# Optimization experiments

Hardware: AMD Instinct MI355X
Metric: run time of the kernel (lower is better)

The kernel has to match this reference:

```python
import jax, jax.numpy as jnp
import numpy as np

E, B, N, F, F1D, H, L, H2, PE_DIM = 4, 16384, 1024, 64, 64, 256, 2, 256, 63
TOPK_MEM = 16      # self.top_K: memory retrieval top-k
W0_SIREN = 30.0    # SIREN omega_0 for 'sine' nonlinearity
NUM_FREQ = 10      # PosEncoding num_frequencies
LINE_DIM = 64      # feat_shapes[0]


def _ln(h, g, b):
    m = jnp.mean(h, axis=-1, keepdims=True)
    v = jnp.mean((h - m) ** 2, axis=-1, keepdims=True)
    return (h - m) / jnp.sqrt(v + 1e-5) * g + b


def _pos_enc(coords):
    # NeRF positional encoding: [coords, sin/cos interleaved per coord per freq]
    freqs = 2.0 ** jnp.arange(NUM_FREQ, dtype=coords.dtype)
    scaled = coords[..., None] * freqs * jnp.pi            # (B, 3, NF)
    sc = jnp.stack([jnp.sin(scaled), jnp.cos(scaled)], axis=-1)  # (B, 3, NF, 2)
    return jnp.concatenate([coords, sc.reshape(coords.shape[0], -1)], axis=-1)  # (B, 63)


def _forward(x, lines, mem_k, mem_v, enc_w0, enc_b0, enc_wh, enc_bh, enc_wo, enc_bo,
             ln_g, ln_b, wq, wk, wv, ad_w0, ad_b0, ad_w1, ad_b1, ad_ln_g, ad_ln_b,
             mg_w0, mg_b0, mg_w1, mg_b1, fw0, fb0, fw1, fb1, fw2, fb2, fw3, fb3, route_k):
    coords = x[:, :3]
    # --- 1D line feature interpolation (param_feats) ---
    p = x[:, 3] * (LINE_DIM - 1)
    pf = jnp.floor(p)
    w = p - pf
    il = pf.astype(jnp.int32)
    ih = jnp.clip(pf + 1.0, 0.0, LINE_DIM - 1).astype(jnp.int32)
    f1d = lines[0][:, il] + w * (lines[0][:, ih] - lines[0][:, il])  # (F1D, B)
    param_feats = f1d.T                                              # (B, F1D)

    pe_x = _pos_enc(coords)                                          # (B, 63)
    scale = float(F) ** 0.5

    def expert(ew0, eb0, ewh, ebh, ewo, ebo, wq_e, wk_e, wv_e, mk, mv,
               aw0, ab0, aw1, ab1, ag, ab):
        # SIREN encoder MLP
        h = jnp.sin(W0_SIREN * (pe_x @ ew0 + eb0))
        for l in range(L):
            h = jnp.sin(W0_SIREN * (h @ ewh[l] + ebh[l]))
        mlp_feats = h @ ewo + ebo                          # (B, F)
        q = _ln(mlp_feats, ln_g, ln_b) @ wq_e              # (B, F)
        kp = mk @ wk_e                                     # (N, F) precomputed keys
        vp = mv @ wv_e                                     # (N, F) precomputed values
        scores = q @ kp.T                                  # (B, N)
        _, idx = jax.lax.top_k(scores, TOPK_MEM)           # (B, K)
        k_top = kp[idx]                                    # (B, K, F)
        v_top = vp[idx]                                    # (B, K, F)
        pfe = jnp.broadcast_to(param_feats[:, None, :], (param_feats.shape[0], TOPK_MEM, F1D))
        a = jnp.concatenate([v_top, pfe], axis=-1)         # (B, K, F+F1D)
        a = jax.nn.relu(a @ aw0 + ab0) @ aw1 + ab1
        adapted = v_top + _ln(a, ag, ab)
        attn = jax.nn.softmax(jnp.einsum('bf,bkf->bk', q, k_top) / scale, axis=-1)
        return jnp.einsum('bk,bkf->bf', attn, adapted) + mlp_feats

    # compute every expert densely (vectorized), then gather routed top-k outputs
    all_out = jax.vmap(expert)(enc_w0, enc_b0, enc_wh, enc_bh, enc_wo, enc_bo,
                               wq, wk, wv, mem_k, mem_v,
                               ad_w0, ad_b0, ad_w1, ad_b1, ad_ln_g, ad_ln_b)  # (E, B, F)

    raw_q = jax.nn.relu(coords @ mg_w0 + mg_b0) @ mg_w1 + mg_b1   # manager_net (B, E)
    probs = jnp.clip(jax.nn.softmax(raw_q, axis=-1), 1e-8, None)
    vals, tidx = jax.lax.top_k(probs, route_k)                    # (B, k)
    vals = vals / jnp.sum(vals, axis=-1, keepdims=True)
    gathered = jnp.take_along_axis(jnp.swapaxes(all_out, 0, 1), tidx[..., None], axis=1)  # (B, k, F)
    spatial = jnp.sum(vals[..., None] * gathered, axis=1)         # (B, F)

    h = jax.nn.relu(spatial @ fw0 + fb0)
    h = jax.nn.relu(h @ fw1 + fb1)
    h = jax.nn.relu(h @ fw2 + fb2)
    refined = jax.nn.sigmoid(h @ fw3 + fb3)
    return refined, raw_q


def setup_inputs() -> dict:
    ks = jax.random.split(jax.random.key(0), 24)
    f32 = jnp.float32
    rn = lambda i, shp, s: jax.random.normal(ks[i], shp, f32) * s
    xav = lambda fi, fo: (2.0 / (fi + fo)) ** 0.5
    return {
        'x': jax.random.uniform(ks[0], (B, 4), f32),
        'lines': jax.random.uniform(ks[1], (1, F1D, LINE_DIM), f32, 0.7, 0.8),
        'mem_k': rn(2, (E, N, F), 1.0),
        'mem_v': rn(3, (E, N, F), 1e-3),
        'enc_w0': rn(4, (E, PE_DIM, H), xav(PE_DIM, H)),
        'enc_b0': jnp.zeros((E, H), f32),
        'enc_wh': rn(5, (E, L, H, H), xav(H, H)),
        'enc_bh': jnp.zeros((E, L, H), f32),
        'enc_wo': rn(6, (E, H, F), xav(H, F)),
        'enc_bo': jnp.zeros((E, F), f32),
        'ln_g': jnp.ones((F,), f32),
        'ln_b': jnp.zeros((F,), f32),
        'wq': rn(7, (E, F, F), xav(F, F)),
        'wk': rn(8, (E, F, F), xav(F, F)),
        'wv': rn(9, (E, F, F), xav(F, F)),
        'ad_w0': rn(10, (E, F + F1D, 64), xav(F + F1D, 64)),
        'ad_b0': rn(11, (E, 64), 1e-3),
        'ad_w1': rn(12, (E, 64, F), xav(64, F)),
        'ad_b1': rn(13, (E, F), 1e-3),
        'ad_ln_g': jnp.ones((E, F), f32),
        'ad_ln_b': jnp.zeros((E, F), f32),
        'mg_w0': rn(14, (3, 64), 0.5),
        'mg_b0': jnp.zeros((64,), f32),
        'mg_w1': rn(15, (64, E), 0.5),
        'mg_b1': jnp.zeros((E,), f32),
        'fw0': rn(16, (F, H2), xav(F, H2)),
        'fb0': rn(17, (H2,), 1e-3),
        'fw1': rn(18, (H2, H2), xav(H2, H2)),
        'fb1': rn(19, (H2,), 1e-3),
        'fw2': rn(20, (H2, H2), xav(H2, H2)),
        'fb2': rn(21, (H2,), 1e-3),
        'fw3': rn(22, (H2, 1), xav(H2, 1)),
        'fb3': rn(23, (1,), 1e-3),
        'route_k': 2,
    }


def reference(x, lines, mem_k, mem_v, enc_w0, enc_b0, enc_wh, enc_bh, enc_wo, enc_bo,
              ln_g, ln_b, wq, wk, wv, ad_w0, ad_b0, ad_w1, ad_b1, ad_ln_g, ad_ln_b,
              mg_w0, mg_b0, mg_w1, mg_b1, fw0, fb0, fw1, fb1, fw2, fb2, fw3, fb3, route_k):
    return _forward(x, lines, mem_k, mem_v, enc_w0, enc_b0, enc_wh, enc_bh, enc_wo, enc_bo,
                    ln_g, ln_b, wq, wk, wv, ad_w0, ad_b0, ad_w1, ad_b1, ad_ln_g, ad_ln_b,
                    mg_w0, mg_b0, mg_w1, mg_b1, fw0, fb0, fw1, fb1, fw2, fb2, fw3, fb3, route_k)
```

## Files before the change

kernel.cpp:

```cpp
#include <hip/hip_runtime.h>
#include <math.h>

#define EE 4
#define BB 16384
#define NN 1024
#define FF 64
#define HH 256
#define PED 63
#define TOPK 16
#define LINE 64
#define TS 32
#define NBX (BB/TS)
#define TSA 64
#define NBA 256

#define OFF_KP   0u
#define OFF_VP   262144u
#define OFF_VPA  524288u
#define OFF_PE   786432u
#define OFF_PF   1818624u
#define OFF_EO   2867200u
#define OFF_RW   4964352u
#define OFF_CNT  4997120u
#define OFF_LIST 4997128u
#define OFF_QV   5062664u
#define OFF_SM   7159816u
#define OFF_WP   OFF_EO

__device__ __forceinline__ float wred_sum(float v) {
#pragma unroll
    for (int off = 32; off > 0; off >>= 1) v += __shfl_xor(v, off, 64);
    return v;
}
__device__ __forceinline__ void wred_sum2(float& a, float& b) {
#pragma unroll
    for (int off = 32; off > 0; off >>= 1) {
        a += __shfl_xor(a, off, 64);
        b += __shfl_xor(b, off, 64);
    }
}

__global__ __launch_bounds__(256) void k_prep(
    const float* __restrict__ wv, const float* __restrict__ aw0,
    float* __restrict__ wp)
{
    int e = blockIdx.x;
    __shared__ float sa[FF*FF];
    for (int i = threadIdx.x; i < FF*FF; i += 256)
        sa[i] = aw0[(size_t)e*128*FF + i];
    __syncthreads();
    int f = threadIdx.x & 63, dg = threadIdx.x >> 6;
    for (int d = dg; d < FF; d += 4) {
        const float* wr = wv + (size_t)e*FF*FF + d*FF;
        float a = 0.f;
        for (int c = 0; c < FF; ++c) a = fmaf(wr[c], sa[c*FF+f], a);
        wp[(size_t)e*FF*FF + d*FF + f] = a;
    }
}

__global__ __launch_bounds__(256) void k_proj(
    const float* __restrict__ mem_k, const float* __restrict__ mem_v,
    const float* __restrict__ wk, const float* __restrict__ wv,
    const float* __restrict__ wp,
    float* __restrict__ kp, float* __restrict__ vp, float* __restrict__ vpa)
{
    int e = blockIdx.x >> 6;
    int nbase = (blockIdx.x & 63) * 16;
    __shared__ float swk[FF*FF], swv[FF*FF], swp[FF*FF];
    for (int i = threadIdx.x; i < FF*FF; i += 256) {
        swk[i] = wk[(size_t)e*FF*FF + i];
        swv[i] = wv[(size_t)e*FF*FF + i];
        swp[i] = wp[(size_t)e*FF*FF + i];
    }
    __syncthreads();
    int r4 = threadIdx.x >> 6;
    int f  = threadIdx.x & 63;
#pragma unroll 1
    for (int it = 0; it < 4; ++it) {
        int n = nbase + it*4 + r4;
        const float* mk = mem_k + ((size_t)e*NN + n)*FF;
        const float* mv = mem_v + ((size_t)e*NN + n)*FF;
        float ak = 0.f, av = 0.f, aa = 0.f;
#pragma unroll 1
        for (int c4 = 0; c4 < 16; ++c4) {
            float4 k4 = *(const float4*)&mk[4*c4];
            float4 v4 = *(const float4*)&mv[4*c4];
#pragma unroll
            for (int kk = 0; kk < 4; ++kk) {
                float mkc = (kk==0)?k4.x:((kk==1)?k4.y:((kk==2)?k4.z:k4.w));
                float mvc = (kk==0)?v4.x:((kk==1)?v4.y:((kk==2)?v4.z:v4.w));
                int c = 4*c4 + kk;
                ak = fmaf(mkc, swk[c*FF+f], ak);
                av = fmaf(mvc, swv[c*FF+f], av);
                aa = fmaf(mvc, swp[c*FF+f], aa);
            }
        }
        kp [((size_t)e*NN+n)*FF + f] = ak;
        vp [((size_t)e*NN+n)*FF + f] = av;
        vpa[((size_t)e*NN+n)*FF + f] = aa;
    }
}

__global__ __launch_bounds__(256) void k_route(
    const float* __restrict__ x, const float* __restrict__ lines,
    const float* __restrict__ mg_w0, const float* __restrict__ mg_b0,
    const float* __restrict__ mg_w1, const float* __restrict__ mg_b1,
    float* __restrict__ pe_x, float* __restrict__ pfm,
    float* __restrict__ rawq, float* __restrict__ rw,
    int* __restrict__ counts, int* __restrict__ lists)
{
    __shared__ float slines[LINE*LINE];
    for (int i = threadIdx.x; i < LINE*LINE; i += 256) slines[i] = lines[i];
    __syncthreads();
    int b = blockIdx.x*256 + threadIdx.x;
    float4 xx = ((const float4*)x)[b];
    float c0 = xx.x, c1 = xx.y, c2 = xx.z, c3 = xx.w;

    float p = c3 * (float)(LINE-1);
    float pfl = floorf(p);
    float w = p - pfl;
    int il = (int)pfl;
    int ih = (int)fminf(fmaxf(pfl + 1.f, 0.f), (float)(LINE-1));
    for (int c = 0; c < FF; ++c) {
        float lo = slines[c*LINE+il], hi = slines[c*LINE+ih];
        pfm[(size_t)b*FF + c] = lo + w*(hi-lo);
    }
    float* pe = pe_x + (size_t)b*PED;
    pe[0]=c0; pe[1]=c1; pe[2]=c2;
    const float PI = 3.14159265358979323846f;
    float coords[3] = {c0,c1,c2};
#pragma unroll
    for (int cc = 0; cc < 3; ++cc) {
        float fr = PI;
        for (int k = 0; k < 10; ++k) {
            float s = coords[cc]*fr;
            pe[3 + cc*20 + k*2 + 0] = sinf(s);
            pe[3 + cc*20 + k*2 + 1] = cosf(s);
            fr *= 2.f;
        }
    }
    float acc[4] = {mg_b1[0], mg_b1[1], mg_b1[2], mg_b1[3]};
    for (int j = 0; j < 64; ++j) {
        float h = fmaf(c0, mg_w0[j], fmaf(c1, mg_w0[64+j], fmaf(c2, mg_w0[128+j], mg_b0[j])));
        h = fmaxf(h, 0.f);
#pragma unroll
        for (int e4 = 0; e4 < 4; ++e4) acc[e4] = fmaf(h, mg_w1[j*4+e4], acc[e4]);
    }
#pragma unroll
    for (int e4 = 0; e4 < 4; ++e4) rawq[(size_t)b*4 + e4] = acc[e4];
    float m = fmaxf(fmaxf(acc[0],acc[1]), fmaxf(acc[2],acc[3]));
    float ex[4], den = 0.f;
#pragma unroll
    for (int e4 = 0; e4 < 4; ++e4) { ex[e4] = expf(acc[e4]-m); den += ex[e4]; }
    float pr[4];
#pragma unroll
    for (int e4 = 0; e4 < 4; ++e4) pr[e4] = fmaxf(ex[e4]/den, 1e-8f);
    int i0 = 0;
#pragma unroll
    for (int e4 = 1; e4 < 4; ++e4) if (pr[e4] > pr[i0]) i0 = e4;
    int i1 = -1;
#pragma unroll
    for (int e4 = 0; e4 < 4; ++e4) {
        if (e4 == i0) continue;
        if (i1 < 0 || pr[e4] > pr[i1]) i1 = e4;
    }
    float vs = pr[i0] + pr[i1];
    rw[b*2+0] = pr[i0]/vs;
    rw[b*2+1] = pr[i1]/vs;
    int p0 = atomicAdd(&counts[i0], 1);
    lists[i0*BB + p0] = b*2 + 0;
    int p1 = atomicAdd(&counts[i1], 1);
    lists[i1*BB + p1] = b*2 + 1;
}

__global__ __launch_bounds__(512, 3) void k_mlp(
    const float* __restrict__ pe_x,
    const float* __restrict__ enc_w0, const float* __restrict__ enc_b0,
    const float* __restrict__ enc_wh, const float* __restrict__ enc_bh,
    const float* __restrict__ enc_wo, const float* __restrict__ enc_bo,
    const float* __restrict__ ln_g, const float* __restrict__ ln_b,
    const float* __restrict__ wq,
    const int* __restrict__ counts, const int* __restrict__ lists,
    float* __restrict__ qv, float* __restrict__ smlpw)
{
    const int e = blockIdx.y;
    const int base = blockIdx.x * TS;
    const int cnt = counts[e];
    if (base >= cnt) return;

    __shared__ float sh[TS*HH];
    __shared__ float swt[4096];
    __shared__ int   slist[TS];

    const int tid = threadIdx.x;
    const int lane = tid & 63;
    const int wv = tid >> 6;
    const int r0 = wv*4;

    if (tid < TS) {
        int idx = base + tid;
        if (idx >= cnt) idx = cnt - 1;
        slist[tid] = lists[e*BB + idx];
    }
    __syncthreads();
    for (int i = tid; i < TS*64; i += 512) {
        int s = i >> 6, j = i & 63;
        int bq = slist[s] >> 1;
        sh[s*HH + j] = (j < PED) ? pe_x[(size_t)bq*PED + j] : 0.f;
    }

    float acc[4][4];

    {
        const float* W = enc_w0 + (size_t)e*PED*HH;
#pragma unroll
        for (int s = 0; s < 4; ++s)
#pragma unroll
            for (int j = 0; j < 4; ++j) acc[s][j] = 0.f;
#pragma unroll 1
        for (int t = 0; t < 4; ++t) {
            int rbase = t*16;
            int rows = (PED - rbase < 16) ? (PED - rbase) : 16;
            int total = rows*HH;
            __syncthreads();
            for (int i = tid*4; i < total; i += 2048)
                *(float4*)&swt[i] = *(const float4*)&W[rbase*HH + i];
            __syncthreads();
#pragma unroll 1
            for (int k = 0; k < rows; ++k) {
                float4 w4 = *(const float4*)&swt[k*HH + 4*lane];
#pragma unroll
                for (int s = 0; s < 4; ++s) {
                    float hv = sh[(r0+s)*HH + rbase + k];
                    acc[s][0] = fmaf(hv, w4.x, acc[s][0]);
                    acc[s][1] = fmaf(hv, w4.y, acc[s][1]);
                    acc[s][2] = fmaf(hv, w4.z, acc[s][2]);
                    acc[s][3] = fmaf(hv, w4.w, acc[s][3]);
                }
            }
        }
        __syncthreads();
        float4 b4 = *(const float4*)&enc_b0[e*HH + 4*lane];
#pragma unroll
        for (int s = 0; s < 4; ++s) {
            float4 o;
            o.x = sinf(30.0f*(acc[s][0] + b4.x));
            o.y = sinf(30.0f*(acc[s][1] + b4.y));
            o.z = sinf(30.0f*(acc[s][2] + b4.z));
            o.w = sinf(30.0f*(acc[s][3] + b4.w));
            *(float4*)&sh[(r0+s)*HH + 4*lane] = o;
        }
    }

#pragma unroll 1
    for (int layer = 0; layer < 2; ++layer) {
        const float* W = enc_wh + ((size_t)(e*2+layer))*HH*HH;
#pragma unroll
        for (int s = 0; s < 4; ++s)
#pragma unroll
            for (int j = 0; j < 4; ++j) acc[s][j] = 0.f;
#pragma unroll 1
        for (int t = 0; t < 16; ++t) {
            __syncthreads();
            for (int i = tid*4; i < 4096; i += 2048)
                *(float4*)&swt[i] = *(const float4*)&W[t*16*HH + i];
            __syncthreads();
#pragma unroll 1
            for (int k4 = 0; k4 < 4; ++k4) {
                float4 h4[4];
#pragma unroll
                for (int s = 0; s < 4; ++s)
                    h4[s] = *(const float4*)&sh[(r0+s)*HH + t*16 + 4*k4];
#pragma unroll
                for (int kk = 0; kk < 4; ++kk) {
                    float4 w4 = *(const float4*)&swt[(4*k4+kk)*HH + 4*lane];
#pragma unroll
                    for (int s = 0; s < 4; ++s) {
                        float hv = (kk==0)?h4[s].x:((kk==1)?h4[s].y:((kk==2)?h4[s].z:h4[s].w));
                        acc[s][0] = fmaf(hv, w4.x, acc[s][0]);
                        acc[s][1] = fmaf(hv, w4.y, acc[s][1]);
                        acc[s][2] = fmaf(hv, w4.z, acc[s][2]);
                        acc[s][3] = fmaf(hv, w4.w, acc[s][3]);
                    }
                }
            }
        }
        __syncthreads();
        float4 b4 = *(const float4*)&enc_bh[(e*2+layer)*HH + 4*lane];
#pragma unroll
        for (int s = 0; s < 4; ++s) {
            float4 o;
            o.x = sinf(30.0f*(acc[s][0] + b4.x));
            o.y = sinf(30.0f*(acc[s][1] + b4.y));
            o.z = sinf(30.0f*(acc[s][2] + b4.z));
            o.w = sinf(30.0f*(acc[s][3] + b4.w));
            *(float4*)&sh[(r0+s)*HH + 4*lane] = o;
        }
    }

    float smlp_r[4];
    {
        const float* W = enc_wo + (size_t)e*HH*FF;
        float a2o[4] = {0.f,0.f,0.f,0.f};
#pragma unroll 1
        for (int t = 0; t < 4; ++t) {
            __syncthreads();
            for (int i = tid*4; i < 4096; i += 2048)
                *(float4*)&swt[i] = *(const float4*)&W[t*64*FF + i];
            __syncthreads();
#pragma unroll 1
            for (int k4 = 0; k4 < 16; ++k4) {
                float4 h4[4];
#pragma unroll
                for (int s = 0; s < 4; ++s)
                    h4[s] = *(const float4*)&sh[(r0+s)*HH + t*64 + 4*k4];
#pragma unroll
                for (int kk = 0; kk < 4; ++kk) {
                    float w = swt[(4*k4+kk)*FF + lane];
#pragma unroll
                    for (int s = 0; s < 4; ++s) {
                        float hv = (kk==0)?h4[s].x:((kk==1)?h4[s].y:((kk==2)?h4[s].z:h4[s].w));
                        a2o[s] = fmaf(hv, w, a2o[s]);
                    }
                }
            }
        }
        float bv = enc_bo[e*FF + lane];
#pragma unroll
        for (int s = 0; s < 4; ++s) smlp_r[s] = a2o[s] + bv;
    }

    {
        const float* Wq = wq + (size_t)e*FF*FF;
        __syncthreads();
        for (int i = tid*4; i < 4096; i += 2048)
            *(float4*)&swt[i] = *(const float4*)&Wq[i];
        __syncthreads();
        float g = ln_g[lane], bb2 = ln_b[lane];
#pragma unroll 1
        for (int s = 0; s < 4; ++s) {
            float hv = smlp_r[s];
            float sm = hv, s2 = hv*hv;
            wred_sum2(sm, s2);
            float mean = sm * (1.f/64.f);
            float var = s2 * (1.f/64.f) - mean*mean;
            float lnv = (hv - mean) * rsqrtf(var + 1e-5f) * g + bb2;
            sh[(r0+s)*HH + lane] = lnv;
            float qa = 0.f;
#pragma unroll 1
            for (int c4 = 0; c4 < 16; ++c4) {
                float4 l4 = *(const float4*)&sh[(r0+s)*HH + 4*c4];
                qa = fmaf(l4.x, swt[(4*c4+0)*FF + lane], qa);
                qa = fmaf(l4.y, swt[(4*c4+1)*FF + lane], qa);
                qa = fmaf(l4.z, swt[(4*c4+2)*FF + lane], qa);
                qa = fmaf(l4.w, swt[(4*c4+3)*FF + lane], qa);
            }
            if (base + r0 + s < cnt) {
                size_t entry = (size_t)slist[r0+s];
                qv[entry*FF + lane] = qa;
                smlpw[entry*FF + lane] = smlp_r[s];
            }
        }
    }
}

__global__ __launch_bounds__(1024, 1) void k_attn(
    const float* __restrict__ pfm,
    const float* __restrict__ kp, const float* __restrict__ vp,
    const float* __restrict__ vpa,
    const float* __restrict__ qv, const float* __restrict__ smlpw,
    const float* __restrict__ aw0, const float* __restrict__ ab0,
    const float* __restrict__ aw1, const float* __restrict__ ab1,
    const float* __restrict__ adg, const float* __restrict__ adb,
    const int* __restrict__ counts, const int* __restrict__ lists,
    float* __restrict__ eo)
{
    const int e = blockIdx.y;
    const int base = blockIdx.x * TSA;
    const int cnt = counts[e];
    if (base >= cnt) return;

    __shared__ float su[16384];
    __shared__ float sa0[4096];
    __shared__ float sw1[4096];
    __shared__ int   slist[TSA];

    float* sq  = su;
    float* skp = su + 4096;

    const int tid = threadIdx.x;
    const int lane = tid & 63;
    const int wv = tid >> 6;
    const int r0 = wv*4;

    if (tid < TSA) {
        int idx = base + tid;
        if (idx >= cnt) idx = cnt - 1;
        slist[tid] = lists[e*BB + idx];
    }
    __syncthreads();
    {
        int s4 = tid >> 4, c4 = (tid & 15)*4;
        *(float4*)&sq[s4*64 + c4] = *(const float4*)&qv[(size_t)slist[s4]*FF + c4];
        const float* a0bG = aw0 + ((size_t)e*128 + 64)*FF;
        const float* w1G  = aw1 + (size_t)e*FF*FF;
        *(float4*)&sa0[tid*4] = *(const float4*)&a0bG[tid*4];
        *(float4*)&sw1[tid*4] = *(const float4*)&w1G[tid*4];
    }

    float sc[4][16];
    {
        const float* kpe = kp + (size_t)e*NN*FF;
        const int str = tid >> 4;
        const int stc = (tid & 15) * 4;
#pragma unroll 1
        for (int c = 0; c < 16; ++c) {
            __syncthreads();
            *(float4*)&skp[str*68 + stc] =
                *(const float4*)&kpe[(size_t)(c*64 + str)*FF + stc];
            __syncthreads();
            float a0 = 0.f, a1 = 0.f, a2s = 0.f, a3 = 0.f;
#pragma unroll
            for (int f4 = 0; f4 < 16; ++f4) {
                float4 k4 = *(const float4*)&skp[lane*68 + 4*f4];
                float4 q0 = *(const float4*)&sq[(r0+0)*64 + 4*f4];
                float4 q1 = *(const float4*)&sq[(r0+1)*64 + 4*f4];
                float4 q2 = *(const float4*)&sq[(r0+2)*64 + 4*f4];
                float4 q3 = *(const float4*)&sq[(r0+3)*64 + 4*f4];
                a0 = fmaf(k4.x,q0.x,fmaf(k4.y,q0.y,fmaf(k4.z,q0.z,fmaf(k4.w,q0.w,a0))));
                a1 = fmaf(k4.x,q1.x,fmaf(k4.y,q1.y,fmaf(k4.z,q1.z,fmaf(k4.w,q1.w,a1))));
                a2s= fmaf(k4.x,q2.x,fmaf(k4.y,q2.y,fmaf(k4.z,q2.z,fmaf(k4.w,q2.w,a2s))));
                a3 = fmaf(k4.x,q3.x,fmaf(k4.y,q3.y,fmaf(k4.z,q3.z,fmaf(k4.w,q3.w,a3))));
            }
            sc[0][c]=a0; sc[1][c]=a1; sc[2][c]=a2s; sc[3][c]=a3;
        }
    }
    __syncthreads();

    const float* vpe  = vp  + (size_t)e*NN*FF;
    const float* vpae = vpa + (size_t)e*NN*FF;
    const float agv = adg[e*FF + lane], abv = adb[e*FF + lane];
    const float ab0v = ab0[e*FF + lane];
    const float ab1v = ab1[e*FF + lane];
    float* plw = &su[wv*1024];

#pragma unroll
    for (int u = 0; u < 4; ++u) {
        int s = r0 + u;
        int entry = slist[s];
        int bq = entry >> 1;

        float pp = ab0v;
        {
            const float* pfr = pfm + (size_t)bq*FF;
#pragma unroll 1
            for (int c4 = 0; c4 < 16; ++c4) {
                float4 p4 = *(const float4*)&pfr[4*c4];
                pp = fmaf(p4.x, sa0[(4*c4+0)*FF + lane], pp);
                pp = fmaf(p4.y, sa0[(4*c4+1)*FF + lane], pp);
                pp = fmaf(p4.z, sa0[(4*c4+2)*FF + lane], pp);
                pp = fmaf(p4.w, sa0[(4*c4+3)*FF + lane], pp);
            }
        }

        int rns[16];
        float wrs[16];
        unsigned taken = 0u;
        bool need = true;
        float bv = -1e30f; int bn = 0x7fffffff;
        float v0max = 0.f, wsum = 0.f;
#pragma unroll
        for (int r = 0; r < TOPK; ++r) {
            if (need) {
                bv = -1e30f; bn = 0x7fffffff;
#pragma unroll
                for (int c = 0; c < 16; ++c) {
                    float v = sc[u][c];
                    int n = c*64 + lane;
                    bool ok = !((taken >> c) & 1u);
                    bool better = ok && (v > bv || (v == bv && n < bn));
                    bv = better ? v : bv;
                    bn = better ? n : bn;
                }
                need = false;
            }
            float rv = bv; int rn = bn;
#pragma unroll
            for (int off = 32; off > 0; off >>= 1) {
                float ov = __shfl_xor(rv, off, 64);
                int on = __shfl_xor(rn, off, 64);
                bool better = (ov > rv) || (ov == rv && on < rn);
                rv = better ? ov : rv;
                rn = better ? on : rn;
            }
            int rn_u = __builtin_amdgcn_readfirstlane(rn);
            if (r == 0) v0max = rv;
            float wr = expf((rv - v0max) * 0.125f);
            wsum += wr;
            if ((rn_u & 63) == lane) { taken |= 1u << (rn_u >> 6); need = true; }
            rns[r] = rn_u;
            wrs[r] = wr;
        }

        float oaccv = 0.f;
#pragma unroll
        for (int g2 = 0; g2 < 2; ++g2) {
            float pav[8], vv[8];
#pragma unroll
            for (int r8 = 0; r8 < 8; ++r8) {
                int r = g2*8 + r8;
                pav[r8] = vpae[(size_t)rns[r]*FF + lane];
                vv[r8]  = vpe [(size_t)rns[r]*FF + lane];
            }
#pragma unroll
            for (int r8 = 0; r8 < 8; ++r8)
                oaccv = fmaf(wrs[g2*8 + r8], vv[r8], oaccv);
#pragma unroll
            for (int q = 0; q < 2; ++q) {
                int qq = g2*2 + q;
                int slot = qq ^ (lane & 3);
                float4 o;
                o.x = fmaxf(pav[4*q+0] + pp, 0.f);
                o.y = fmaxf(pav[4*q+1] + pp, 0.f);
                o.z = fmaxf(pav[4*q+2] + pp, 0.f);
                o.w = fmaxf(pav[4*q+3] + pp, 0.f);
                *(float4*)&plw[lane*16 + slot*4] = o;
            }
        }
        float a2[16];
#pragma unroll
        for (int r = 0; r < 16; ++r) a2[r] = ab1v;
#pragma unroll 1
        for (int j4 = 0; j4 < 16; ++j4) {
            const float* plj = &plw[j4*64];
#pragma unroll
            for (int jj = 0; jj < 4; ++jj) {
                float w = sw1[(4*j4+jj)*FF + lane];
#pragma unroll
                for (int lq = 0; lq < 4; ++lq) {
                    float4 d = *(const float4*)&plj[jj*16 + ((lq ^ jj) * 4)];
                    a2[4*lq+0] = fmaf(d.x, w, a2[4*lq+0]);
                    a2[4*lq+1] = fmaf(d.y, w, a2[4*lq+1]);
                    a2[4*lq+2] = fmaf(d.z, w, a2[4*lq+2]);
                    a2[4*lq+3] = fmaf(d.w, w, a2[4*lq+3]);
                }
            }
        }
        float oln = 0.f;
#pragma unroll
        for (int r = 0; r < TOPK; ++r) {
            float av = a2[r];
            float sm = av, s2 = av*av;
            wred_sum2(sm, s2);
            float mean = sm * (1.f/64.f);
            float var = s2 * (1.f/64.f) - mean*mean;
            float lnv = (av - mean) * rsqrtf(var + 1e-5f) * agv + abv;
            oln = fmaf(wrs[r], lnv, oln);
        }
        float res = (oaccv + oln) / wsum + smlpw[(size_t)entry*FF + lane];
        if (base + s < cnt) eo[(size_t)entry*FF + lane] = res;
    }
}

__global__ __launch_bounds__(512, 3) void k_final(
    const float* __restrict__ eo, const float* __restrict__ rw,
    const float* __restrict__ fw0, const float* __restrict__ fb0,
    const float* __restrict__ fw1, const float* __restrict__ fb1,
    const float* __restrict__ fw2, const float* __restrict__ fb2,
    const float* __restrict__ fw3, const float* __restrict__ fb3,
    float* __restrict__ refined)
{
    __shared__ float sh[TS*HH];
    __shared__ float swt[4096];
    const int tid = threadIdx.x, lane = tid & 63, wv = tid >> 6;
    const int sbase = blockIdx.x * TS;
    const int r0 = wv*4;
    for (int i = tid; i < TS*64; i += 512) {
        int s = i >> 6, c = i & 63;
        int b = sbase + s;
        sh[s*HH + c] = rw[b*2]*eo[(size_t)(b*2)*FF + c]
                     + rw[b*2+1]*eo[(size_t)(b*2+1)*FF + c];
    }
    float acc[4][4];
    {
#pragma unroll
        for (int s = 0; s < 4; ++s)
#pragma unroll
            for (int j = 0; j < 4; ++j) acc[s][j] = 0.f;
#pragma unroll 1
        for (int t = 0; t < 4; ++t) {
            __syncthreads();
            for (int i = tid*4; i < 4096; i += 2048)
                *(float4*)&swt[i] = *(const float4*)&fw0[t*16*HH + i];
            __syncthreads();
#pragma unroll 1
            for (int k = 0; k < 16; ++k) {
                float4 w4 = *(const float4*)&swt[k*HH + 4*lane];
#pragma unroll
                for (int s = 0; s < 4; ++s) {
                    float hv = sh[(r0+s)*HH + t*16 + k];
                    acc[s][0] = fmaf(hv, w4.x, acc[s][0]);
                    acc[s][1] = fmaf(hv, w4.y, acc[s][1]);
                    acc[s][2] = fmaf(hv, w4.z, acc[s][2]);
                    acc[s][3] = fmaf(hv, w4.w, acc[s][3]);
                }
            }
        }
        __syncthreads();
        float4 b4 = *(const float4*)&fb0[4*lane];
#pragma unroll
        for (int s = 0; s < 4; ++s) {
            float4 o;
            o.x = fmaxf(acc[s][0] + b4.x, 0.f);
            o.y = fmaxf(acc[s][1] + b4.y, 0.f);
            o.z = fmaxf(acc[s][2] + b4.z, 0.f);
            o.w = fmaxf(acc[s][3] + b4.w, 0.f);
            *(float4*)&sh[(r0+s)*HH + 4*lane] = o;
        }
    }
#pragma unroll 1
    for (int layer = 0; layer < 2; ++layer) {
        const float* W  = layer ? fw2 : fw1;
        const float* bi = layer ? fb2 : fb1;
#pragma unroll
        for (int s = 0; s < 4; ++s)
#pragma unroll
            for (int j = 0; j < 4; ++j) acc[s][j] = 0.f;
#pragma unroll 1
        for (int t = 0; t < 16; ++t) {
            __syncthreads();
            for (int i = tid*4; i < 4096; i += 2048)
                *(float4*)&swt[i] = *(const float4*)&W[t*16*HH + i];
            __syncthreads();
#pragma unroll 1
            for (int k4 = 0; k4 < 4; ++k4) {
                float4 h4[4];
#pragma unroll
                for (int s = 0; s < 4; ++s)
                    h4[s] = *(const float4*)&sh[(r0+s)*HH + t*16 + 4*k4];
#pragma unroll
                for (int kk = 0; kk < 4; ++kk) {
                    float4 w4 = *(const float4*)&swt[(4*k4+kk)*HH + 4*lane];
#pragma unroll
                    for (int s = 0; s < 4; ++s) {
                        float hv = (kk==0)?h4[s].x:((kk==1)?h4[s].y:((kk==2)?h4[s].z:h4[s].w));
                        acc[s][0] = fmaf(hv, w4.x, acc[s][0]);
                        acc[s][1] = fmaf(hv, w4.y, acc[s][1]);
                        acc[s][2] = fmaf(hv, w4.z, acc[s][2]);
                        acc[s][3] = fmaf(hv, w4.w, acc[s][3]);
                    }
                }
            }
        }
        __syncthreads();
        float4 b4 = *(const float4*)&bi[4*lane];
#pragma unroll
        for (int s = 0; s < 4; ++s) {
            float4 o;
            o.x = fmaxf(acc[s][0] + b4.x, 0.f);
            o.y = fmaxf(acc[s][1] + b4.y, 0.f);
            o.z = fmaxf(acc[s][2] + b4.z, 0.f);
            o.w = fmaxf(acc[s][3] + b4.w, 0.f);
            *(float4*)&sh[(r0+s)*HH + 4*lane] = o;
        }
    }
    {
        float4 w4 = *(const float4*)&fw3[4*lane];
#pragma unroll 1
        for (int s = 0; s < 4; ++s) {
            float4 h4 = *(const float4*)&sh[(r0+s)*HH + 4*lane];
            float part = h4.x*w4.x + h4.y*w4.y + h4.z*w4.z + h4.w*w4.w;
            float tot = wred_sum(part) + fb3[0];
            float r = 1.f/(1.f + expf(-tot));
            if (lane == 0) refined[sbase + r0 + s] = r;
        }
    }
}

extern "C" void kernel_launch(void* const* d_in, const int* in_sizes, int n_in,
                              void* d_out, int out_size, void* d_ws, size_t ws_size,
                              hipStream_t stream)
{
    const float* x      = (const float*)d_in[0];
    const float* lines  = (const float*)d_in[1];
    const float* mem_k  = (const float*)d_in[2];
    const float* mem_v  = (const float*)d_in[3];
    const float* enc_w0 = (const float*)d_in[4];
    const float* enc_b0 = (const float*)d_in[5];
    const float* enc_wh = (const float*)d_in[6];
    const float* enc_bh = (const float*)d_in[7];
    const float* enc_wo = (const float*)d_in[8];
    const float* enc_bo = (const float*)d_in[9];
    const float* ln_g   = (const float*)d_in[10];
    const float* ln_b   = (const float*)d_in[11];
    const float* wq     = (const float*)d_in[12];
    const float* wk     = (const float*)d_in[13];
    const float* wv_    = (const float*)d_in[14];
    const float* ad_w0  = (const float*)d_in[15];
    const float* ad_b0  = (const float*)d_in[16];
    const float* ad_w1  = (const float*)d_in[17];
    const float* ad_b1  = (const float*)d_in[18];
    const float* ad_g   = (const float*)d_in[19];
    const float* ad_b   = (const float*)d_in[20];
    const float* mg_w0  = (const float*)d_in[21];
    const float* mg_b0  = (const float*)d_in[22];
    const float* mg_w1  = (const float*)d_in[23];
    const float* mg_b1  = (const float*)d_in[24];
    const float* fw0    = (const float*)d_in[25];
    const float* fb0    = (const float*)d_in[26];
    const float* fw1    = (const float*)d_in[27];
    const float* fb1    = (const float*)d_in[28];
    const float* fw2    = (const float*)d_in[29];
    const float* fb2    = (const float*)d_in[30];
    const float* fw3    = (const float*)d_in[31];
    const float* fb3    = (const float*)d_in[32];

    float* out_ref = (float*)d_out;
    float* out_rq  = (float*)d_out + BB;

    float* ws  = (float*)d_ws;
    float* kp  = ws + OFF_KP;
    float* vp  = ws + OFF_VP;
    float* vpa = ws + OFF_VPA;
    float* pe  = ws + OFF_PE;
    float* pfm = ws + OFF_PF;
    float* eo  = ws + OFF_EO;
    float* rw  = ws + OFF_RW;
    float* qvw = ws + OFF_QV;
    float* smw = ws + OFF_SM;
    float* wpw = ws + OFF_WP;
    int*  cnts = (int*)(ws + OFF_CNT);
    int*  lst  = (int*)(ws + OFF_LIST);

    hipMemsetAsync(cnts, 0, EE*sizeof(int), stream);
    k_prep<<<dim3(EE), dim3(256), 0, stream>>>(wv_, ad_w0, wpw);
    k_proj<<<dim3(EE*64), dim3(256), 0, stream>>>(mem_k, mem_v, wk, wv_, wpw, kp, vp, vpa);
    k_route<<<dim3(BB/256), dim3(256), 0, stream>>>(x, lines, mg_w0, mg_b0, mg_w1, mg_b1,
                                                    pe, pfm, out_rq, rw, cnts, lst);
    k_mlp<<<dim3(NBX, EE), dim3(512), 0, stream>>>(pe,
        enc_w0, enc_b0, enc_wh, enc_bh, enc_wo, enc_bo, ln_g, ln_b, wq,
        cnts, lst, qvw, smw);
    k_attn<<<dim3(NBA, EE), dim3(1024), 0, stream>>>(pfm, kp, vp, vpa, qvw, smw,
        ad_w0, ad_b0, ad_w1, ad_b1, ad_g, ad_b, cnts, lst, eo);
    k_final<<<dim3(BB/TS), dim3(512), 0, stream>>>(eo, rw, fw0, fb0, fw1, fb1,
                                                   fw2, fb2, fw3, fb3, out_ref);
}
```

Measured before the change: 1.469 ms.

## Halve attention tile to 32 rows and keep top-k indices in lanes

Result: faster. 1.268 ms (-13.7%).

```diff
diff --git a/kernel.cpp b/kernel.cpp
--- a/kernel.cpp
+++ b/kernel.cpp
@@ -11,8 +11,7 @@
 #define LINE 64
 #define TS 32
 #define NBX (BB/TS)
-#define TSA 64
-#define NBA 256
+#define TSA2 32
 
 #define OFF_KP   0u
 #define OFF_VP   262144u
@@ -364,7 +363,7 @@
     }
 }
 
-__global__ __launch_bounds__(1024, 1) void k_attn(
+__global__ __launch_bounds__(1024) void k_attn(
     const float* __restrict__ pfm,
     const float* __restrict__ kp, const float* __restrict__ vp,
     const float* __restrict__ vpa,
@@ -376,39 +375,40 @@
     float* __restrict__ eo)
 {
     const int e = blockIdx.y;
-    const int base = blockIdx.x * TSA;
+    const int base = blockIdx.x * TSA2;
     const int cnt = counts[e];
     if (base >= cnt) return;
 
+    __shared__ float sq[TSA2*FF];
     __shared__ float su[16384];
     __shared__ float sa0[4096];
     __shared__ float sw1[4096];
-    __shared__ int   slist[TSA];
-
-    float* sq  = su;
-    float* skp = su + 4096;
+    __shared__ int   slist[TSA2];
 
     const int tid = threadIdx.x;
     const int lane = tid & 63;
     const int wv = tid >> 6;
-    const int r0 = wv*4;
-
-    if (tid < TSA) {
+    const int r0 = wv*2;
+
+    if (tid < TSA2) {
         int idx = base + tid;
         if (idx >= cnt) idx = cnt - 1;
         slist[tid] = lists[e*BB + idx];
     }
     __syncthreads();
-    {
+    if (tid < 512) {
         int s4 = tid >> 4, c4 = (tid & 15)*4;
         *(float4*)&sq[s4*64 + c4] = *(const float4*)&qv[(size_t)slist[s4]*FF + c4];
+    }
+    {
         const float* a0bG = aw0 + ((size_t)e*128 + 64)*FF;
         const float* w1G  = aw1 + (size_t)e*FF*FF;
         *(float4*)&sa0[tid*4] = *(const float4*)&a0bG[tid*4];
         *(float4*)&sw1[tid*4] = *(const float4*)&w1G[tid*4];
     }
 
-    float sc[4][16];
+    float sc[2][16];
+    float* skp = su;
     {
         const float* kpe = kp + (size_t)e*NN*FF;
         const int str = tid >> 4;
@@ -419,20 +419,16 @@
             *(float4*)&skp[str*68 + stc] =
                 *(const float4*)&kpe[(size_t)(c*64 + str)*FF + stc];
             __syncthreads();
-            float a0 = 0.f, a1 = 0.f, a2s = 0.f, a3 = 0.f;
+            float a0 = 0.f, a1 = 0.f;
 #pragma unroll
             for (int f4 = 0; f4 < 16; ++f4) {
                 float4 k4 = *(const float4*)&skp[lane*68 + 4*f4];
                 float4 q0 = *(const float4*)&sq[(r0+0)*64 + 4*f4];
                 float4 q1 = *(const float4*)&sq[(r0+1)*64 + 4*f4];
-                float4 q2 = *(const float4*)&sq[(r0+2)*64 + 4*f4];
-                float4 q3 = *(const float4*)&sq[(r0+3)*64 + 4*f4];
                 a0 = fmaf(k4.x,q0.x,fmaf(k4.y,q0.y,fmaf(k4.z,q0.z,fmaf(k4.w,q0.w,a0))));
                 a1 = fmaf(k4.x,q1.x,fmaf(k4.y,q1.y,fmaf(k4.z,q1.z,fmaf(k4.w,q1.w,a1))));
-                a2s= fmaf(k4.x,q2.x,fmaf(k4.y,q2.y,fmaf(k4.z,q2.z,fmaf(k4.w,q2.w,a2s))));
-                a3 = fmaf(k4.x,q3.x,fmaf(k4.y,q3.y,fmaf(k4.z,q3.z,fmaf(k4.w,q3.w,a3))));
-            }
-            sc[0][c]=a0; sc[1][c]=a1; sc[2][c]=a2s; sc[3][c]=a3;
+            }
+            sc[0][c]=a0; sc[1][c]=a1;
         }
     }
     __syncthreads();
@@ -445,7 +441,7 @@
     float* plw = &su[wv*1024];
 
 #pragma unroll
-    for (int u = 0; u < 4; ++u) {
+    for (int u = 0; u < 2; ++u) {
         int s = r0 + u;
         int entry = slist[s];
         int bq = entry >> 1;
@@ -463,8 +459,7 @@
             }
         }
 
-        int rns[16];
-        float wrs[16];
+        float wr_my = 0.f; int rn_my = 0;
         unsigned taken = 0u;
         bool need = true;
         float bv = -1e30f; int bn = 0x7fffffff;
@@ -493,39 +488,33 @@
                 rv = better ? ov : rv;
                 rn = better ? on : rn;
             }
-            int rn_u = __builtin_amdgcn_readfirstlane(rn);
             if (r == 0) v0max = rv;
             float wr = expf((rv - v0max) * 0.125f);
             wsum += wr;
-            if ((rn_u & 63) == lane) { taken |= 1u << (rn_u >> 6); need = true; }
-            rns[r] = rn_u;
-            wrs[r] = wr;
+            if ((rn & 63) == lane) { taken |= 1u << (rn >> 6); need = true; }
+            if (lane == r) { wr_my = wr; rn_my = rn; }
         }
 
         float oaccv = 0.f;
 #pragma unroll
-        for (int g2 = 0; g2 < 2; ++g2) {
-            float pav[8], vv[8];
-#pragma unroll
-            for (int r8 = 0; r8 < 8; ++r8) {
-                int r = g2*8 + r8;
-                pav[r8] = vpae[(size_t)rns[r]*FF + lane];
-                vv[r8]  = vpe [(size_t)rns[r]*FF + lane];
-            }
-#pragma unroll
-            for (int r8 = 0; r8 < 8; ++r8)
-                oaccv = fmaf(wrs[g2*8 + r8], vv[r8], oaccv);
-#pragma unroll
-            for (int q = 0; q < 2; ++q) {
-                int qq = g2*2 + q;
-                int slot = qq ^ (lane & 3);
-                float4 o;
-                o.x = fmaxf(pav[4*q+0] + pp, 0.f);
-                o.y = fmaxf(pav[4*q+1] + pp, 0.f);
-                o.z = fmaxf(pav[4*q+2] + pp, 0.f);
-                o.w = fmaxf(pav[4*q+3] + pp, 0.f);
-                *(float4*)&plw[lane*16 + slot*4] = o;
-            }
+        for (int b4i = 0; b4i < 4; ++b4i) {
+            float pav4[4];
+#pragma unroll
+            for (int j = 0; j < 4; ++j) {
+                int r = b4i*4 + j;
+                int rn_b = __shfl(rn_my, r, 64);
+                float wr_b = __shfl(wr_my, r, 64);
+                pav4[j] = vpae[(size_t)rn_b*FF + lane];
+                float vv = vpe[(size_t)rn_b*FF + lane];
+                oaccv = fmaf(wr_b, vv, oaccv);
+            }
+            int slot = b4i ^ (lane & 3);
+            float4 o;
+            o.x = fmaxf(pav4[0] + pp, 0.f);
+            o.y = fmaxf(pav4[1] + pp, 0.f);
+            o.z = fmaxf(pav4[2] + pp, 0.f);
+            o.w = fmaxf(pav4[3] + pp, 0.f);
+            *(float4*)&plw[lane*16 + slot*4] = o;
         }
         float a2[16];
 #pragma unroll
@@ -555,7 +544,8 @@
             float mean = sm * (1.f/64.f);
             float var = s2 * (1.f/64.f) - mean*mean;
             float lnv = (av - mean) * rsqrtf(var + 1e-5f) * agv + abv;
-            oln = fmaf(wrs[r], lnv, oln);
+            float wr_b = __shfl(wr_my, r, 64);
+            oln = fmaf(wr_b, lnv, oln);
         }
         float res = (oaccv + oln) / wsum + smlpw[(size_t)entry*FF + lane];
         if (base + s < cnt) eo[(size_t)entry*FF + lane] = res;
@@ -740,7 +730,7 @@
     k_mlp<<<dim3(NBX, EE), dim3(512), 0, stream>>>(pe,
         enc_w0, enc_b0, enc_wh, enc_bh, enc_wo, enc_bo, ln_g, ln_b, wq,
         cnts, lst, qvw, smw);
-    k_attn<<<dim3(NBA, EE), dim3(1024), 0, stream>>>(pfm, kp, vp, vpa, qvw, smw,
+    k_attn<<<dim3(BB/TSA2, EE), dim3(1024), 0, stream>>>(pfm, kp, vp, vpa, qvw, smw,
         ad_w0, ad_b0, ad_w1, ad_b1, ad_g, ad_b, cnts, lst, eo);
     k_final<<<dim3(BB/TS), dim3(512), 0, stream>>>(eo, rw, fw0, fb0, fw1, fb1,
                                                    fw2, fb2, fw3, fb3, out_ref);
```
